# Kernel tuning notes

Hardware: AMD Instinct MI355X
Metric: run time of the kernel (lower is better)

Reference implementation:

```python
import jax, jax.numpy as jnp
import numpy as np

N = 100000   # nodes
E = 1600000  # edges (avg in-degree 16)
D = 64       # feature dim (dim_in = dim_out)


def setup_inputs() -> dict:
    key = jax.random.key(0)
    k1, k2, k3, k4, k5, k6 = jax.random.split(key, 6)
    h = jax.random.normal(k1, (N, D), dtype=jnp.float32)
    src = jax.random.randint(k2, (E,), 0, N, dtype=jnp.int32)
    dst = jax.random.randint(k3, (E,), 0, N, dtype=jnp.int32)
    scale = 1.0 / np.sqrt(D).astype(np.float32)
    W1 = jax.random.normal(k4, (D, D), dtype=jnp.float32) * scale  # Linear(dim_in, dim_out, bias=False)
    W2 = jax.random.normal(k5, (D, D), dtype=jnp.float32) * scale  # Linear(dim_out, dim_out, bias=True)
    b2 = jax.random.normal(k6, (D,), dtype=jnp.float32) * scale
    return {"h": h, "src": src, "dst": dst, "W1": W1, "W2": W2, "b2": b2}


def reference(h, src, dst, W1, W2, b2):
    # GINConv with 'max' aggregation, eps = 0 (DGL default, not learned):
    #   out = MLP( h + max_{(u->v) in E} h[u] )
    msgs = h[src]  # [E, D] gather of source features
    agg = jax.ops.segment_max(msgs, dst, num_segments=N)  # [N, D]
    # Nodes with no in-edges: DGL's max-reduce yields zeros, segment_max yields -inf.
    deg = jax.ops.segment_sum(jnp.ones((E,), dtype=h.dtype), dst, num_segments=N)  # [N]
    agg = jnp.where(deg[:, None] > 0, agg, jnp.zeros((), dtype=h.dtype))
    x = h + agg                       # (1 + eps) * h_dst + agg, eps = 0
    y = jnp.maximum(x @ W1.T, 0.0)    # Linear(no bias) + ReLU
    return y @ W2.T + b2              # Linear(bias)
```

## Files before the change

### kernel.cpp

```cpp
#include <hip/hip_runtime.h>
#include <math.h>

#define NN 100000
#define EE 1600000
#define D 64

#define BSH 7
#define BSIZE 128
#define NBUK ((NN + BSIZE - 1) / BSIZE)
#define CAP 2296
#define EPB 8192
#define SCATB ((EE + EPB - 1) / EPB)
#define AST 65


__device__ __forceinline__ unsigned short encbf(float x) {
    unsigned int b = __float_as_uint(x);
    unsigned short u = (unsigned short)((b + 0x7FFFu + ((b >> 16) & 1u)) >> 16);
    return u ^ ((u & 0x8000u) ? 0xFFFFu : 0x8000u);
}

__device__ __forceinline__ unsigned int pkmax(unsigned int a, unsigned int b) {
    unsigned int d;
    asm("v_pk_max_u16 %0, %1, %2" : "=v"(d) : "v"(a), "v"(b));
    return d;
}

__global__ void __launch_bounds__(256) kAP(const float* __restrict__ h,
                                           unsigned short* __restrict__ hb,
                                           const float* __restrict__ W1, float* __restrict__ W1T,
                                           const float* __restrict__ W2, float* __restrict__ W2T,
                                           const int* __restrict__ src, const int* __restrict__ dst,
                                           int* __restrict__ gcur, int* __restrict__ bdata) {
    __shared__ int lcnt[NBUK];
    __shared__ int lcur[NBUK];
    const int t = threadIdx.x;
    const int b = blockIdx.x;
    if (b < SCATB) {
        for (int i = t; i < NBUK; i += 256) lcnt[i] = 0;
        __syncthreads();
        const int e0 = b * EPB;
        int dc[32];
#pragma unroll
        for (int k = 0; k < 32; k++) {
            int e = e0 + k * 256 + t;
            int d = -1;
            if (e < EE) {
                d = dst[e];
                atomicAdd(&lcnt[d >> BSH], 1);
            }
            dc[k] = d;
        }
        __syncthreads();
        for (int i = t; i < NBUK; i += 256)
            if (lcnt[i]) lcur[i] = atomicAdd(&gcur[i], lcnt[i]);
        __syncthreads();
#pragma unroll
        for (int k = 0; k < 32; k++) {
            int e = e0 + k * 256 + t;
            if (e < EE) {
                int d2 = dc[k];
                int bk = d2 >> BSH;
                int pos = atomicAdd(&lcur[bk], 1);
                if (pos < CAP) bdata[bk * CAP + pos] = (src[e] << BSH) | (d2 & (BSIZE - 1));
            }
        }
    }
    int gi = b * 256 + t;
    const float4* h4 = (const float4*)h;
    ushort4* hb4 = (ushort4*)hb;
    for (int idx = gi; idx < NN * D / 4; idx += gridDim.x * 256) {
        float4 v = h4[idx];
        ushort4 r;
        r.x = encbf(v.x); r.y = encbf(v.y); r.z = encbf(v.z); r.w = encbf(v.w);
        hb4[idx] = r;
    }
    if (gi < D * D) {
        int k = gi >> 6, j = gi & 63;
        W1T[gi] = W1[j * D + k];
        W2T[gi] = W2[j * D + k];
    }
}

__global__ void __launch_bounds__(512) kC2(const float* __restrict__ h,
                                           const unsigned short* __restrict__ hb,
                                           const int* __restrict__ gcur,
                                           const int* __restrict__ bdata,
                                           const float* __restrict__ W1T,
                                           const float* __restrict__ W2T,
                                           const float* __restrict__ b2,
                                           float* __restrict__ out) {
    __shared__ unsigned int acc[BSIZE * AST];
    __shared__ int deg[BSIZE];
    __shared__ int scn[BSIZE];
    __shared__ int cur[BSIZE];
    float* fac = (float*)acc;
    unsigned int* elist = acc;
    const int t = threadIdx.x;
    const int b = blockIdx.x;
    int cnt = gcur[b];
    if (cnt > CAP) cnt = CAP;
    const int base = b * CAP;

    if (t < BSIZE) deg[t] = 0;
    __syncthreads();
    for (int i = t; i < cnt; i += 512)
        atomicAdd(&deg[bdata[base + i] & (BSIZE - 1)], 1);
    __syncthreads();
    if (t < BSIZE) scn[t] = deg[t];
    __syncthreads();
    for (int s = 1; s < BSIZE; s <<= 1) {
        int v = 0;
        if (t < BSIZE) { v = scn[t]; if (t >= s) v += scn[t - s]; }
        __syncthreads();
        if (t < BSIZE) scn[t] = v;
        __syncthreads();
    }
    if (t < BSIZE) cur[t] = scn[t] - deg[t];
    __syncthreads();
    for (int i = t; i < cnt; i += 512) {
        int e = bdata[base + i];
        int pos = atomicAdd(&cur[e & (BSIZE - 1)], 1);
        elist[pos] = ((unsigned)e) >> BSH;
    }
    __syncthreads();

    const int wave = t >> 6, lane = t & 63;
    const int oct = lane >> 3;
    const int fbyte = (lane & 7) * 16;
    const char* hbB = (const char*)hb;
    unsigned int m[2][4];
#pragma unroll
    for (int p = 0; p < 2; ++p)
#pragma unroll
        for (int c = 0; c < 4; ++c) m[p][c] = 0u;

#pragma unroll
    for (int p = 0; p < 2; ++p) {
        const int n8 = wave * 16 + p * 8 + oct;
        const int dg = deg[n8];
        const int of = scn[n8] - deg[n8];
        int md = dg;
        md = max(md, __shfl_xor(md, 8));
        md = max(md, __shfl_xor(md, 16));
        md = max(md, __shfl_xor(md, 32));
#pragma unroll 4
        for (int r = 0; r < md; ++r) {
            if (r < dg) {
                unsigned int sidx = elist[of + r];
                const uint4 uu = *(const uint4*)(hbB + (size_t)sidx * 128 + fbyte);
                m[p][0] = pkmax(m[p][0], uu.x);
                m[p][1] = pkmax(m[p][1], uu.y);
                m[p][2] = pkmax(m[p][2], uu.z);
                m[p][3] = pkmax(m[p][3], uu.w);
            }
        }
    }
    __syncthreads();

#pragma unroll
    for (int p = 0; p < 2; ++p) {
        const int n8 = wave * 16 + p * 8 + oct;
        const int v = b * BSIZE + n8;
        const int f0 = (lane & 7) * 8;
        float x[8];
#pragma unroll
        for (int c = 0; c < 4; ++c) {
            unsigned int w = m[p][c];
            unsigned int klo = w & 0xFFFFu;
            unsigned int khi = w >> 16;
            float mlo = 0.0f, mhi = 0.0f;
            if (klo) {
                unsigned int bb = (klo & 0x8000u) ? (klo ^ 0x8000u) : ((~klo) & 0xFFFFu);
                mlo = __uint_as_float(bb << 16);
            }
            if (khi) {
                unsigned int bb = (khi & 0x8000u) ? (khi ^ 0x8000u) : ((~khi) & 0xFFFFu);
                mhi = __uint_as_float(bb << 16);
            }
            x[2 * c] = mlo;
            x[2 * c + 1] = mhi;
        }
        if (v < NN) {
            const float4* hp = (const float4*)(h + (size_t)v * D + f0);
            float4 a0 = hp[0], a1 = hp[1];
            x[0] += a0.x; x[1] += a0.y; x[2] += a0.z; x[3] += a0.w;
            x[4] += a1.x; x[5] += a1.y; x[6] += a1.z; x[7] += a1.w;
        } else {
#pragma unroll
            for (int j = 0; j < 8; ++j) x[j] = 0.0f;
        }
#pragma unroll
        for (int j = 0; j < 8; ++j) fac[n8 * AST + f0 + j] = x[j];
    }
    __syncthreads();

    const int n = t & (BSIZE - 1);
    const int hq = __builtin_amdgcn_readfirstlane(t >> 7);
    const float* w1 = W1T + hq * 16;
    const float* w2 = W2T + hq * 16;
    float y[16];
#pragma unroll
    for (int jj = 0; jj < 16; jj++) y[jj] = 0.0f;
#pragma unroll 8
    for (int k = 0; k < D; k++) {
        float xk = fac[n * AST + k];
#pragma unroll
        for (int jj = 0; jj < 16; jj++)
            y[jj] = fmaf(xk, w1[k * D + jj], y[jj]);
    }
#pragma unroll
    for (int jj = 0; jj < 16; jj++) y[jj] = fmaxf(y[jj], 0.0f);
    __syncthreads();
#pragma unroll
    for (int jj = 0; jj < 16; jj++) fac[n * AST + hq * 16 + jj] = y[jj];
    __syncthreads();

    float o[16];
#pragma unroll
    for (int ii = 0; ii < 16; ii++) o[ii] = b2[hq * 16 + ii];
#pragma unroll 8
    for (int j = 0; j < D; j++) {
        float yj = fac[n * AST + j];
#pragma unroll
        for (int ii = 0; ii < 16; ii++)
            o[ii] = fmaf(yj, w2[j * D + ii], o[ii]);
    }
    int v = b * BSIZE + n;
    if (v < NN) {
        float4* op = (float4*)(out + (size_t)v * D + hq * 16);
#pragma unroll
        for (int c = 0; c < 4; c++)
            op[c] = make_float4(o[4 * c], o[4 * c + 1], o[4 * c + 2], o[4 * c + 3]);
    }
}

extern "C" void kernel_launch(void* const* d_in, const int* in_sizes, int n_in,
                              void* d_out, int out_size, void* d_ws, size_t ws_size,
                              hipStream_t stream) {
    const float* h   = (const float*)d_in[0];
    const int*   src = (const int*)d_in[1];
    const int*   dst = (const int*)d_in[2];
    const float* W1  = (const float*)d_in[3];
    const float* W2  = (const float*)d_in[4];
    const float* b2  = (const float*)d_in[5];
    float* out = (float*)d_out;

    int* ws = (int*)d_ws;
    int* gcur  = ws;
    int* bdata = ws + 784;
    float* W2T = (float*)(ws + 784 + NBUK * CAP);
    float* W1T = W2T + D * D;
    unsigned short* hb = (unsigned short*)(W1T + D * D);

    hipMemsetAsync(gcur, 0, 784 * sizeof(int), stream);
    kAP<<<1024, 256, 0, stream>>>(h, hb, W1, W1T, W2, W2T, src, dst, gcur, bdata);
    kC2<<<NBUK, 512, 0, stream>>>(h, hb, gcur, bdata, W1T, W2T, b2, out);
}
```

Baseline: 194.2 us.

## Replace bucketed scatter and bf16 gather with per-node fixed-slot adjacency in fp32

Drops the two-level bucket scatter (block-local histograms, then an in-kernel counting sort) and the bf16 order-preserving encoding of h. Each edge now does a global atomic on a per-node counter and writes its source id into a fixed 48-slot row for that node. The aggregation kernel copies the slot array straight into LDS and gathers fp32 rows with 4-way batched loads and fmaxf. This removes the sort and the conversion pass, but doubles gather bytes and adds 1.6M global atomics on contended counters. Any node with more than 48 in-edges is silently truncated, which risks wrong results.

```diff
diff --git a/kernel.cpp b/kernel.cpp
--- a/kernel.cpp
+++ b/kernel.cpp
@@ -5,154 +5,98 @@
 #define EE 1600000
 #define D 64
 
+#define PCAP 48
 #define BSH 7
 #define BSIZE 128
 #define NBUK ((NN + BSIZE - 1) / BSIZE)
-#define CAP 2296
-#define EPB 8192
-#define SCATB ((EE + EPB - 1) / EPB)
 #define AST 65
 
 
-__device__ __forceinline__ unsigned short encbf(float x) {
-    unsigned int b = __float_as_uint(x);
-    unsigned short u = (unsigned short)((b + 0x7FFFu + ((b >> 16) & 1u)) >> 16);
-    return u ^ ((u & 0x8000u) ? 0xFFFFu : 0x8000u);
-}
-
-__device__ __forceinline__ unsigned int pkmax(unsigned int a, unsigned int b) {
-    unsigned int d;
-    asm("v_pk_max_u16 %0, %1, %2" : "=v"(d) : "v"(a), "v"(b));
-    return d;
-}
-
-__global__ void __launch_bounds__(256) kAP(const float* __restrict__ h,
-                                           unsigned short* __restrict__ hb,
-                                           const float* __restrict__ W1, float* __restrict__ W1T,
-                                           const float* __restrict__ W2, float* __restrict__ W2T,
-                                           const int* __restrict__ src, const int* __restrict__ dst,
-                                           int* __restrict__ gcur, int* __restrict__ bdata) {
-    __shared__ int lcnt[NBUK];
-    __shared__ int lcur[NBUK];
-    const int t = threadIdx.x;
-    const int b = blockIdx.x;
-    if (b < SCATB) {
-        for (int i = t; i < NBUK; i += 256) lcnt[i] = 0;
-        __syncthreads();
-        const int e0 = b * EPB;
-        int dc[32];
-#pragma unroll
-        for (int k = 0; k < 32; k++) {
-            int e = e0 + k * 256 + t;
-            int d = -1;
-            if (e < EE) {
-                d = dst[e];
-                atomicAdd(&lcnt[d >> BSH], 1);
-            }
-            dc[k] = d;
-        }
-        __syncthreads();
-        for (int i = t; i < NBUK; i += 256)
-            if (lcnt[i]) lcur[i] = atomicAdd(&gcur[i], lcnt[i]);
-        __syncthreads();
-#pragma unroll
-        for (int k = 0; k < 32; k++) {
-            int e = e0 + k * 256 + t;
-            if (e < EE) {
-                int d2 = dc[k];
-                int bk = d2 >> BSH;
-                int pos = atomicAdd(&lcur[bk], 1);
-                if (pos < CAP) bdata[bk * CAP + pos] = (src[e] << BSH) | (d2 & (BSIZE - 1));
-            }
-        }
+__global__ void __launch_bounds__(256) kScat(const int* __restrict__ src,
+                                             const int* __restrict__ dst,
+                                             int* __restrict__ cur,
+                                             int* __restrict__ bdata,
+                                             const float* __restrict__ W1, float* __restrict__ W1T,
+                                             const float* __restrict__ W2, float* __restrict__ W2T) {
+    const int gid = blockIdx.x * 256 + threadIdx.x;
+    const int gsz = gridDim.x * 256;
+    for (int e = gid; e < EE; e += gsz) {
+        int v = dst[e];
+        int pos = atomicAdd(&cur[v], 1);
+        if (pos < PCAP) bdata[v * PCAP + pos] = src[e];
     }
-    int gi = b * 256 + t;
-    const float4* h4 = (const float4*)h;
-    ushort4* hb4 = (ushort4*)hb;
-    for (int idx = gi; idx < NN * D / 4; idx += gridDim.x * 256) {
-        float4 v = h4[idx];
-        ushort4 r;
-        r.x = encbf(v.x); r.y = encbf(v.y); r.z = encbf(v.z); r.w = encbf(v.w);
-        hb4[idx] = r;
-    }
-    if (gi < D * D) {
-        int k = gi >> 6, j = gi & 63;
-        W1T[gi] = W1[j * D + k];
-        W2T[gi] = W2[j * D + k];
+    if (gid < D * D) {
+        int k = gid >> 6, j = gid & 63;
+        W1T[gid] = W1[j * D + k];
+        W2T[gid] = W2[j * D + k];
     }
 }
 
-__global__ void __launch_bounds__(512) kC2(const float* __restrict__ h,
-                                           const unsigned short* __restrict__ hb,
-                                           const int* __restrict__ gcur,
-                                           const int* __restrict__ bdata,
-                                           const float* __restrict__ W1T,
-                                           const float* __restrict__ W2T,
-                                           const float* __restrict__ b2,
-                                           float* __restrict__ out) {
+__global__ void __launch_bounds__(512, 4) kC3(const float* __restrict__ h,
+                                              const int* __restrict__ cur,
+                                              const int* __restrict__ bdata,
+                                              const float* __restrict__ W1T,
+                                              const float* __restrict__ W2T,
+                                              const float* __restrict__ b2,
+                                              float* __restrict__ out) {
     __shared__ unsigned int acc[BSIZE * AST];
     __shared__ int deg[BSIZE];
-    __shared__ int scn[BSIZE];
-    __shared__ int cur[BSIZE];
     float* fac = (float*)acc;
-    unsigned int* elist = acc;
+    int* elist = (int*)acc;
     const int t = threadIdx.x;
     const int b = blockIdx.x;
-    int cnt = gcur[b];
-    if (cnt > CAP) cnt = CAP;
-    const int base = b * CAP;
 
-    if (t < BSIZE) deg[t] = 0;
-    __syncthreads();
-    for (int i = t; i < cnt; i += 512)
-        atomicAdd(&deg[bdata[base + i] & (BSIZE - 1)], 1);
-    __syncthreads();
-    if (t < BSIZE) scn[t] = deg[t];
-    __syncthreads();
-    for (int s = 1; s < BSIZE; s <<= 1) {
-        int v = 0;
-        if (t < BSIZE) { v = scn[t]; if (t >= s) v += scn[t - s]; }
-        __syncthreads();
-        if (t < BSIZE) scn[t] = v;
-        __syncthreads();
+    if (t < BSIZE) {
+        int v = b * BSIZE + t;
+        int dgv = (v < NN) ? cur[v] : 0;
+        deg[t] = dgv > PCAP ? PCAP : dgv;
     }
-    if (t < BSIZE) cur[t] = scn[t] - deg[t];
-    __syncthreads();
-    for (int i = t; i < cnt; i += 512) {
-        int e = bdata[base + i];
-        int pos = atomicAdd(&cur[e & (BSIZE - 1)], 1);
-        elist[pos] = ((unsigned)e) >> BSH;
-    }
+    const int ebase = b * (BSIZE * PCAP);
+    for (int i = t; i < BSIZE * PCAP; i += 512) elist[i] = bdata[ebase + i];
     __syncthreads();
 
     const int wave = t >> 6, lane = t & 63;
     const int oct = lane >> 3;
-    const int fbyte = (lane & 7) * 16;
-    const char* hbB = (const char*)hb;
-    unsigned int m[2][4];
+    const int f0 = (lane & 7) * 8;
+    float m[2][8];
 #pragma unroll
     for (int p = 0; p < 2; ++p)
 #pragma unroll
-        for (int c = 0; c < 4; ++c) m[p][c] = 0u;
+        for (int j = 0; j < 8; ++j) m[p][j] = -INFINITY;
 
 #pragma unroll
     for (int p = 0; p < 2; ++p) {
         const int n8 = wave * 16 + p * 8 + oct;
         const int dg = deg[n8];
-        const int of = scn[n8] - deg[n8];
+        const int ofs = n8 * PCAP;
         int md = dg;
         md = max(md, __shfl_xor(md, 8));
         md = max(md, __shfl_xor(md, 16));
         md = max(md, __shfl_xor(md, 32));
-#pragma unroll 4
-        for (int r = 0; r < md; ++r) {
-            if (r < dg) {
-                unsigned int sidx = elist[of + r];
-                const uint4 uu = *(const uint4*)(hbB + (size_t)sidx * 128 + fbyte);
-                m[p][0] = pkmax(m[p][0], uu.x);
-                m[p][1] = pkmax(m[p][1], uu.y);
-                m[p][2] = pkmax(m[p][2], uu.z);
-                m[p][3] = pkmax(m[p][3], uu.w);
+        for (int r0 = 0; r0 < md; r0 += 4) {
+            float4 ua[4], ub[4];
+#pragma unroll
+            for (int g = 0; g < 4; ++g) {
+                int r = r0 + g;
+                ua[g] = make_float4(-INFINITY, -INFINITY, -INFINITY, -INFINITY);
+                ub[g] = ua[g];
+                if (r < dg) {
+                    int sidx = elist[ofs + r];
+                    const float4* hp = (const float4*)(h + (size_t)sidx * D + f0);
+                    ua[g] = hp[0];
+                    ub[g] = hp[1];
+                }
+            }
+#pragma unroll
+            for (int g = 0; g < 4; ++g) {
+                m[p][0] = fmaxf(m[p][0], ua[g].x);
+                m[p][1] = fmaxf(m[p][1], ua[g].y);
+                m[p][2] = fmaxf(m[p][2], ua[g].z);
+                m[p][3] = fmaxf(m[p][3], ua[g].w);
+                m[p][4] = fmaxf(m[p][4], ub[g].x);
+                m[p][5] = fmaxf(m[p][5], ub[g].y);
+                m[p][6] = fmaxf(m[p][6], ub[g].z);
+                m[p][7] = fmaxf(m[p][7], ub[g].w);
             }
         }
     }
@@ -162,30 +106,17 @@
     for (int p = 0; p < 2; ++p) {
         const int n8 = wave * 16 + p * 8 + oct;
         const int v = b * BSIZE + n8;
-        const int f0 = (lane & 7) * 8;
+        const int dg = deg[n8];
         float x[8];
-#pragma unroll
-        for (int c = 0; c < 4; ++c) {
-            unsigned int w = m[p][c];
-            unsigned int klo = w & 0xFFFFu;
-            unsigned int khi = w >> 16;
-            float mlo = 0.0f, mhi = 0.0f;
-            if (klo) {
-                unsigned int bb = (klo & 0x8000u) ? (klo ^ 0x8000u) : ((~klo) & 0xFFFFu);
-                mlo = __uint_as_float(bb << 16);
-            }
-            if (khi) {
-                unsigned int bb = (khi & 0x8000u) ? (khi ^ 0x8000u) : ((~khi) & 0xFFFFu);
-                mhi = __uint_as_float(bb << 16);
-            }
-            x[2 * c] = mlo;
-            x[2 * c + 1] = mhi;
-        }
         if (v < NN) {
             const float4* hp = (const float4*)(h + (size_t)v * D + f0);
             float4 a0 = hp[0], a1 = hp[1];
-            x[0] += a0.x; x[1] += a0.y; x[2] += a0.z; x[3] += a0.w;
-            x[4] += a1.x; x[5] += a1.y; x[6] += a1.z; x[7] += a1.w;
+            x[0] = a0.x; x[1] = a0.y; x[2] = a0.z; x[3] = a0.w;
+            x[4] = a1.x; x[5] = a1.y; x[6] = a1.z; x[7] = a1.w;
+            if (dg > 0) {
+#pragma unroll
+                for (int j = 0; j < 8; ++j) x[j] += m[p][j];
+            }
         } else {
 #pragma unroll
             for (int j = 0; j < 8; ++j) x[j] = 0.0f;
@@ -247,13 +178,12 @@
     float* out = (float*)d_out;
 
     int* ws = (int*)d_ws;
-    int* gcur  = ws;
-    int* bdata = ws + 784;
-    float* W2T = (float*)(ws + 784 + NBUK * CAP);
-    float* W1T = W2T + D * D;
-    unsigned short* hb = (unsigned short*)(W1T + D * D);
+    int* cur   = ws;
+    int* bdata = ws + NN;
+    float* W1T = (float*)(ws + NN + NN * PCAP);
+    float* W2T = W1T + D * D;
 
-    hipMemsetAsync(gcur, 0, 784 * sizeof(int), stream);
-    kAP<<<1024, 256, 0, stream>>>(h, hb, W1, W1T, W2, W2T, src, dst, gcur, bdata);
-    kC2<<<NBUK, 512, 0, stream>>>(h, hb, gcur, bdata, W1T, W2T, b2, out);
+    hipMemsetAsync(cur, 0, NN * sizeof(int), stream);
+    kScat<<<1024, 256, 0, stream>>>(src, dst, cur, bdata, W1, W1T, W2, W2T);
+    kC3<<<NBUK, 512, 0, stream>>>(h, cur, bdata, W1T, W2T, b2, out);
 }
```

Result: slower. 301.5 us (+55.2%).
